# Optimization experiments

Measured on AMD Instinct MI355X. Metric: run time of the kernel, lower is better.

Reference implementation:

```python
import jax, jax.numpy as jnp
import numpy as np

B, N, INP = 16, 1024, 256
HEADS, DIM_HEAD = 8, 32
INNER = HEADS * DIM_HEAD  # 256
OUP = 256
IH = IW = 32  # IH*IW == N


def _relative_index(ih, iw):
    # mirrors the torch __init__ construction (meshgrid indexing='ij')
    coords = np.stack(np.meshgrid(np.arange(ih), np.arange(iw), indexing='ij')).reshape(2, -1)
    rel = coords[:, :, None] - coords[:, None, :]  # [2, N, N]
    rel[0] += ih - 1
    rel[1] += iw - 1
    rel[0] *= 2 * iw - 1
    return rel.sum(0).reshape(-1)  # [N*N]


def setup_inputs() -> dict:
    key = jax.random.key(0)
    kx, kqkv, kout, kbias = jax.random.split(key, 4)
    x = jax.random.normal(kx, (B, N, INP), dtype=jnp.float32)
    w_qkv = jax.random.normal(kqkv, (INP, 3 * INNER), dtype=jnp.float32) * 0.02
    w_out = jax.random.normal(kout, (INNER, OUP), dtype=jnp.float32) * 0.02
    b_out = jnp.zeros((OUP,), dtype=jnp.float32)
    bias_table = jax.random.normal(kbias, ((2 * IH - 1) * (2 * IW - 1), HEADS), dtype=jnp.float32) * 0.02
    relative_index = jnp.asarray(_relative_index(IH, IW), dtype=jnp.int32)
    return {"x": x, "w_qkv": w_qkv, "w_out": w_out, "b_out": b_out,
            "bias_table": bias_table, "relative_index": relative_index}


def reference(x, w_qkv, w_out, b_out, bias_table, relative_index):
    b, n, _ = x.shape
    scale = DIM_HEAD ** (-0.5)
    qkv = x @ w_qkv  # [b, n, 3*inner]
    q, k, v = jnp.split(qkv, 3, axis=-1)
    split_heads = lambda t: t.reshape(b, n, HEADS, DIM_HEAD).transpose(0, 2, 1, 3)  # b h n d
    q, k, v = split_heads(q), split_heads(k), split_heads(v)
    dots = jnp.einsum('bhnd,bhmd->bhnm', q, k) * scale  # [b, h, n, n]
    # gather bias: (n*n, heads) -> (1, heads, n, n), matching '(h w) c -> 1 c h w'
    rel_bias = bias_table[relative_index].reshape(n, n, HEADS).transpose(2, 0, 1)[None]
    attn = jax.nn.softmax(dots + rel_bias, axis=-1)
    out = jnp.einsum('bhnm,bhmd->bhnd', attn, v)
    out = out.transpose(0, 2, 1, 3).reshape(b, n, INNER)  # b n (h d)
    return out @ w_out + b_out
```

## Files before the change

kernel.cpp:

```cpp
#include <hip/hip_runtime.h>
#include <hip/hip_bf16.h>

typedef __bf16 bf16;
typedef bf16 bf16x4 __attribute__((ext_vector_type(4)));
typedef bf16 bf16x8 __attribute__((ext_vector_type(8)));
typedef float f32x4 __attribute__((ext_vector_type(4)));

#define MFMA32(A, B, C) __builtin_amdgcn_mfma_f32_16x16x32_bf16(A, B, C, 0, 0, 0)
#define GL2LDS16(gp, lp)                                                            \
  __builtin_amdgcn_global_load_lds((const __attribute__((address_space(1))) unsigned int*)(gp), \
                                   (__attribute__((address_space(3))) unsigned int*)(lp), 16, 0, 0)

static constexpr float SCALE = 0.17677669529663687f;
static constexpr float LOG2E = 1.4426950408889634f;

__global__ __launch_bounds__(256) void k_prep(const float* __restrict__ x,
                                              const float* __restrict__ wqkv,
                                              const float* __restrict__ wout,
                                              const float* __restrict__ table,
                                              const int* __restrict__ ridx,
                                              bf16* __restrict__ xb, bf16* __restrict__ wtq,
                                              bf16* __restrict__ wto, bf16* __restrict__ rbb) {
  const int tid = threadIdx.x;
  const int blk = blockIdx.x;
  if (blk < 2048) {
    int t = blk * 256 + tid;
    const float4* s = reinterpret_cast<const float4*>(x) + (size_t)t * 2;
    float4 a = s[0], c = s[1];
    bf16x8 o;
    o[0] = (bf16)a.x; o[1] = (bf16)a.y; o[2] = (bf16)a.z; o[3] = (bf16)a.w;
    o[4] = (bf16)c.x; o[5] = (bf16)c.y; o[6] = (bf16)c.z; o[7] = (bf16)c.w;
    reinterpret_cast<bf16x8*>(xb)[t] = o;
  } else if (blk < 3072) {
    int t = (blk - 2048) * 256 + tid;
    if (t < 196608) {
      int n = t >> 8, k = t & 255;
      wtq[t] = (bf16)wqkv[k * 768 + n];
    } else {
      int t2 = t - 196608;
      int n = t2 >> 8, k = t2 & 255;
      wto[t2] = (bf16)wout[k * 256 + n];
    }
  } else {
    const int bb2 = blk - 3072;
    const int qt = bb2 >> 6, kt = bb2 & 63;
    const int r = tid & 3, lane = tid >> 2;
    const int ln = lane & 15, quad = lane >> 4;
    const int qrow = qt * 16 + ln;
    const int key = kt * 16 + quad * 4 + r;
    const int idx = ridx[qrow * 1024 + key];
    const float4* p = reinterpret_cast<const float4*>(table) + idx * 2;
    float4 a = p[0], c = p[1];
    float vals[8] = {a.x, a.y, a.z, a.w, c.x, c.y, c.z, c.w};
    const int base = bb2 * 256 + tid;
#pragma unroll
    for (int h = 0; h < 8; ++h) rbb[h * 1048576 + base] = (bf16)(vals[h] * LOG2E);
  }
}

template <int EPI>
__global__ __launch_bounds__(256) void k_gemm(const bf16* __restrict__ A,
                                              const bf16* __restrict__ Bt,
                                              bf16* __restrict__ q, bf16* __restrict__ kk,
                                              bf16* __restrict__ vt, float* __restrict__ out,
                                              const float* __restrict__ bout) {
  __shared__ __align__(16) bf16 As[128 * 40];
  __shared__ __align__(16) bf16 Bs[128 * 40];
  const int tid = threadIdx.x;
  const int ln = tid & 15, quad = (tid >> 4) & 3, wv = tid >> 6;
  const int wm = (wv >> 1) * 64, wn = (wv & 1) * 64;
  const int m0 = blockIdx.x * 128, n0 = blockIdx.y * 128;
  const int srow = tid >> 2, scg = (tid & 3) * 8;
  f32x4 acc[4][4] = {};

  for (int kt = 0; kt < 256; kt += 32) {
    bf16x8 av0 = *reinterpret_cast<const bf16x8*>(&A[(m0 + srow) * 256 + kt + scg]);
    bf16x8 av1 = *reinterpret_cast<const bf16x8*>(&A[(m0 + 64 + srow) * 256 + kt + scg]);
    bf16x8 bv0 = *reinterpret_cast<const bf16x8*>(&Bt[(n0 + srow) * 256 + kt + scg]);
    bf16x8 bv1 = *reinterpret_cast<const bf16x8*>(&Bt[(n0 + 64 + srow) * 256 + kt + scg]);
    *reinterpret_cast<bf16x8*>(&As[srow * 40 + scg]) = av0;
    *reinterpret_cast<bf16x8*>(&As[(64 + srow) * 40 + scg]) = av1;
    *reinterpret_cast<bf16x8*>(&Bs[srow * 40 + scg]) = bv0;
    *reinterpret_cast<bf16x8*>(&Bs[(64 + srow) * 40 + scg]) = bv1;
    __syncthreads();
    bf16x8 af[4], bfr[4];
#pragma unroll
    for (int i = 0; i < 4; ++i)
      af[i] = *reinterpret_cast<const bf16x8*>(&As[(wm + i * 16 + ln) * 40 + quad * 8]);
#pragma unroll
    for (int i = 0; i < 4; ++i)
      bfr[i] = *reinterpret_cast<const bf16x8*>(&Bs[(wn + i * 16 + ln) * 40 + quad * 8]);
#pragma unroll
    for (int i = 0; i < 4; ++i)
#pragma unroll
      for (int j = 0; j < 4; ++j) acc[i][j] = MFMA32(af[i], bfr[j], acc[i][j]);
    __syncthreads();
  }

  if (EPI == 0) {
    const int colbase = n0 + wn;
    const int seg = colbase >> 8;
    const int cb = colbase & 255;
    const float mul = (seg == 0) ? SCALE * LOG2E : 1.0f;
#pragma unroll
    for (int i = 0; i < 4; ++i) {
      const int gm = m0 + wm + i * 16 + quad * 4;
      const int b = gm >> 10;
#pragma unroll
      for (int j = 0; j < 4; ++j) {
        const int gc = cb + j * 16 + ln;
        const int h = gc >> 5, d = gc & 31;
#pragma unroll
        for (int r = 0; r < 4; ++r) {
          const int nseq = (gm + r) & 1023;
          if (seg == 2) {
            const int p6 = nseq & 63;
            const int c6 = ((p6 >> 2) & 3) * 16 + (p6 >> 4) * 4 + (p6 & 3);
            const int kcol = (nseq & ~63) | c6;
            vt[(b * 8 + h) * 32768 + d * 1024 + kcol] = (bf16)acc[i][j][r];
          } else {
            bf16* dst = (seg == 0) ? q : kk;
            dst[(b * 8 + h) * 32768 + nseq * 32 + d] = (bf16)(acc[i][j][r] * mul);
          }
        }
      }
    }
  } else {
#pragma unroll
    for (int j = 0; j < 4; ++j) {
      const int gc = n0 + wn + j * 16 + ln;
      const float bb = bout[gc];
#pragma unroll
      for (int i = 0; i < 4; ++i) {
        const int gm = m0 + wm + i * 16 + quad * 4;
#pragma unroll
        for (int r = 0; r < 4; ++r) out[(size_t)(gm + r) * 256 + gc] = acc[i][j][r] + bb;
      }
    }
  }
}

__global__ __launch_bounds__(256) void k_flash(const bf16* __restrict__ qs,
                                               const bf16* __restrict__ ks,
                                               const bf16* __restrict__ vtg,
                                               const bf16* __restrict__ rbb,
                                               bf16* __restrict__ ao) {
  __shared__ __align__(16) bf16 Ks[2][2048];
  __shared__ __align__(16) bf16 Vs[2][2048];
  __shared__ __align__(16) bf16 Ps[4][16][72];
  const int tid = threadIdx.x;
  const int lane = tid & 63;
  const int ln = lane & 15, quad = lane >> 4, wv = tid >> 6;
  const int blk = blockIdx.x;
  const int bh = blk & 127;
  const int b = bh >> 3, h = bh & 7;
  const int qtw = (blk >> 7) * 4 + wv;
  const int q0 = qtw * 16;
  const bf16* qb = qs + bh * 32768;
  const bf16* kb = ks + bh * 32768;
  const bf16* vb = vtg + bh * 32768;
  const bf16* bbias = rbb + h * 1048576 + qtw * 16384 + lane * 4;

  const bf16* kg = kb + lane * 32 + wv * 8;
  const bf16* vg = vb + (lane & 31) * 1024 + (wv * 2 + (lane >> 5)) * 8;
  bf16* kls0 = &Ks[0][wv * 512];
  bf16* vls0 = &Vs[0][wv * 512];
  bf16* kls1 = &Ks[1][wv * 512];
  bf16* vls1 = &Vs[1][wv * 512];

  const bf16x8 qfrag = *reinterpret_cast<const bf16x8*>(&qb[(q0 + ln) * 32 + quad * 8]);

  f32x4 acc0 = {0.f, 0.f, 0.f, 0.f}, acc1 = {0.f, 0.f, 0.f, 0.f};
  float lsum = 0.f;

  bf16x4 cbf[2][4];
#pragma unroll
  for (int nt = 0; nt < 4; ++nt) cbf[0][nt] = *reinterpret_cast<const bf16x4*>(&bbias[nt * 256]);
  GL2LDS16(kg, kls0);
  GL2LDS16(vg, vls0);

#pragma unroll 2
  for (int it = 0; it < 16; ++it) {
    const int cur = it & 1, nxt = cur ^ 1;
    const int k0 = it * 64;
    __syncthreads();
    const int kpf = (it < 15) ? k0 + 64 : k0;
    GL2LDS16(kg + kpf * 32, cur ? kls0 : kls1);
    GL2LDS16(vg + kpf, cur ? vls0 : vls1);
#pragma unroll
    for (int nt = 0; nt < 4; ++nt)
      cbf[nxt][nt] = *reinterpret_cast<const bf16x4*>(&bbias[((it < 15 ? it + 1 : it) * 4 + nt) * 256]);
    bf16x8 kf[4];
#pragma unroll
    for (int nt = 0; nt < 4; ++nt)
      kf[nt] = *reinterpret_cast<const bf16x8*>(&Ks[cur][quad * 512 + (nt * 16 + ln) * 8]);
    f32x4 s[4];
#pragma unroll
    for (int nt = 0; nt < 4; ++nt) {
      f32x4 c;
#pragma unroll
      for (int e = 0; e < 4; ++e) c[e] = (float)cbf[cur][nt][e];
      s[nt] = MFMA32(kf[nt], qfrag, c);
    }
    bf16x8 va0 = *reinterpret_cast<const bf16x8*>(&Vs[cur][quad * 256 + ln * 8]);
    bf16x8 vc0 = *reinterpret_cast<const bf16x8*>(&Vs[cur][quad * 256 + (16 + ln) * 8]);
    bf16x8 va1 = *reinterpret_cast<const bf16x8*>(&Vs[cur][(4 + quad) * 256 + ln * 8]);
    bf16x8 vc1 = *reinterpret_cast<const bf16x8*>(&Vs[cur][(4 + quad) * 256 + (16 + ln) * 8]);
#pragma unroll
    for (int nt = 0; nt < 4; ++nt)
#pragma unroll
      for (int e = 0; e < 4; ++e) s[nt][e] = __builtin_amdgcn_exp2f(s[nt][e]);
#pragma unroll
    for (int nt = 0; nt < 4; ++nt) lsum += (s[nt][0] + s[nt][1]) + (s[nt][2] + s[nt][3]);
    bf16x8 lo, hi;
#pragma unroll
    for (int e = 0; e < 4; ++e) {
      lo[e] = (bf16)s[0][e];
      lo[4 + e] = (bf16)s[1][e];
      hi[e] = (bf16)s[2][e];
      hi[4 + e] = (bf16)s[3][e];
    }
    *reinterpret_cast<bf16x8*>(&Ps[wv][ln][quad * 16]) = lo;
    *reinterpret_cast<bf16x8*>(&Ps[wv][ln][quad * 16 + 8]) = hi;
    bf16x8 pa0 = *reinterpret_cast<const bf16x8*>(&Ps[wv][ln][quad * 8]);
    bf16x8 pa1 = *reinterpret_cast<const bf16x8*>(&Ps[wv][ln][32 + quad * 8]);
    acc0 = MFMA32(pa0, va0, acc0);
    acc1 = MFMA32(pa0, vc0, acc1);
    acc0 = MFMA32(pa1, va1, acc0);
    acc1 = MFMA32(pa1, vc1, acc1);
  }

  lsum += __shfl_xor(lsum, 16, 64);
  lsum += __shfl_xor(lsum, 32, 64);

#pragma unroll
  for (int r = 0; r < 4; ++r) {
    const float inv = __builtin_amdgcn_rcpf(__shfl(lsum, quad * 4 + r, 64));
    const int row = q0 + quad * 4 + r;
    bf16* po = &ao[(size_t)(b * 1024 + row) * 256 + h * 32 + ln];
    po[0] = (bf16)(acc0[r] * inv);
    po[16] = (bf16)(acc1[r] * inv);
  }
}

extern "C" void kernel_launch(void* const* d_in, const int* in_sizes, int n_in,
                              void* d_out, int out_size, void* d_ws, size_t ws_size,
                              hipStream_t stream) {
  const float* x = (const float*)d_in[0];
  const float* wqkv = (const float*)d_in[1];
  const float* wout = (const float*)d_in[2];
  const float* bout = (const float*)d_in[3];
  const float* btab = (const float*)d_in[4];
  const int* ridx = (const int*)d_in[5];
  float* out = (float*)d_out;

  char* ws = (char*)d_ws;
  bf16* xb  = (bf16*)(ws + 0);
  bf16* wtq = (bf16*)(ws + 8388608);
  bf16* wto = (bf16*)(ws + 8781824);
  bf16* q   = (bf16*)(ws + 8912896);
  bf16* k   = (bf16*)(ws + 17301504);
  bf16* vt  = (bf16*)(ws + 25690112);
  bf16* rb  = (bf16*)(ws + 34078720);
  bf16* ao  = (bf16*)(ws + 50855936);

  k_prep<<<7168, 256, 0, stream>>>(x, wqkv, wout, btab, ridx, xb, wtq, wto, rb);
  k_gemm<0><<<dim3(128, 6), 256, 0, stream>>>(xb, wtq, q, k, vt, nullptr, nullptr);
  k_flash<<<2048, 256, 0, stream>>>(q, k, vt, rb, ao);
  k_gemm<1><<<dim3(128, 2), 256, 0, stream>>>(ao, wto, nullptr, nullptr, nullptr, out, bout);
}
```

Before: 159.5 us.

## Double-buffer GEMM via direct global-to-LDS loads; process two query tiles per flash wave

The GEMM kernel now stages A/B tiles with global_load_lds into double-buffered shared memory without padding. This removes one barrier per step and overlaps the next tile's load with the MFMAs. The flash kernel has each wave handle two 16-row query tiles, so each K/V shared-memory fragment is reused twice, and the grid is halved. The changes raise register pressure and may add LDS bank conflicts in the unpadded GEMM layout, and the smaller grid reduces parallelism.

```diff
diff --git a/kernel.cpp b/kernel.cpp
--- a/kernel.cpp
+++ b/kernel.cpp
@@ -64,37 +64,43 @@
                                               bf16* __restrict__ q, bf16* __restrict__ kk,
                                               bf16* __restrict__ vt, float* __restrict__ out,
                                               const float* __restrict__ bout) {
-  __shared__ __align__(16) bf16 As[128 * 40];
-  __shared__ __align__(16) bf16 Bs[128 * 40];
+  __shared__ __align__(16) bf16 As[2][4096];
+  __shared__ __align__(16) bf16 Bs[2][4096];
   const int tid = threadIdx.x;
   const int ln = tid & 15, quad = (tid >> 4) & 3, wv = tid >> 6;
   const int wm = (wv >> 1) * 64, wn = (wv & 1) * 64;
   const int m0 = blockIdx.x * 128, n0 = blockIdx.y * 128;
   const int srow = tid >> 2, scg = (tid & 3) * 8;
+  const bf16* ag = A + (size_t)(m0 + srow) * 256 + scg;
+  const bf16* bg = Bt + (size_t)(n0 + srow) * 256 + scg;
   f32x4 acc[4][4] = {};
 
+  GL2LDS16(ag, &As[0][tid * 8]);
+  GL2LDS16(ag + 64 * 256, &As[0][2048 + tid * 8]);
+  GL2LDS16(bg, &Bs[0][tid * 8]);
+  GL2LDS16(bg + 64 * 256, &Bs[0][2048 + tid * 8]);
+
+#pragma unroll 2
   for (int kt = 0; kt < 256; kt += 32) {
-    bf16x8 av0 = *reinterpret_cast<const bf16x8*>(&A[(m0 + srow) * 256 + kt + scg]);
-    bf16x8 av1 = *reinterpret_cast<const bf16x8*>(&A[(m0 + 64 + srow) * 256 + kt + scg]);
-    bf16x8 bv0 = *reinterpret_cast<const bf16x8*>(&Bt[(n0 + srow) * 256 + kt + scg]);
-    bf16x8 bv1 = *reinterpret_cast<const bf16x8*>(&Bt[(n0 + 64 + srow) * 256 + kt + scg]);
-    *reinterpret_cast<bf16x8*>(&As[srow * 40 + scg]) = av0;
-    *reinterpret_cast<bf16x8*>(&As[(64 + srow) * 40 + scg]) = av1;
-    *reinterpret_cast<bf16x8*>(&Bs[srow * 40 + scg]) = bv0;
-    *reinterpret_cast<bf16x8*>(&Bs[(64 + srow) * 40 + scg]) = bv1;
+    const int cur = (kt >> 5) & 1, nxt = cur ^ 1;
     __syncthreads();
+    if (kt < 224) {
+      GL2LDS16(ag + kt + 32, &As[nxt][tid * 8]);
+      GL2LDS16(ag + 64 * 256 + kt + 32, &As[nxt][2048 + tid * 8]);
+      GL2LDS16(bg + kt + 32, &Bs[nxt][tid * 8]);
+      GL2LDS16(bg + 64 * 256 + kt + 32, &Bs[nxt][2048 + tid * 8]);
+    }
     bf16x8 af[4], bfr[4];
 #pragma unroll
     for (int i = 0; i < 4; ++i)
-      af[i] = *reinterpret_cast<const bf16x8*>(&As[(wm + i * 16 + ln) * 40 + quad * 8]);
+      af[i] = *reinterpret_cast<const bf16x8*>(&As[cur][(wm + i * 16 + ln) * 32 + quad * 8]);
 #pragma unroll
     for (int i = 0; i < 4; ++i)
-      bfr[i] = *reinterpret_cast<const bf16x8*>(&Bs[(wn + i * 16 + ln) * 40 + quad * 8]);
+      bfr[i] = *reinterpret_cast<const bf16x8*>(&Bs[cur][(wn + i * 16 + ln) * 32 + quad * 8]);
 #pragma unroll
     for (int i = 0; i < 4; ++i)
 #pragma unroll
       for (int j = 0; j < 4; ++j) acc[i][j] = MFMA32(af[i], bfr[j], acc[i][j]);
-    __syncthreads();
   }
 
   if (EPI == 0) {
@@ -147,37 +153,39 @@
                                                bf16* __restrict__ ao) {
   __shared__ __align__(16) bf16 Ks[2][2048];
   __shared__ __align__(16) bf16 Vs[2][2048];
-  __shared__ __align__(16) bf16 Ps[4][16][72];
+  __shared__ __align__(16) bf16 Ps[4][2][16][72];
   const int tid = threadIdx.x;
   const int lane = tid & 63;
   const int ln = lane & 15, quad = lane >> 4, wv = tid >> 6;
   const int blk = blockIdx.x;
   const int bh = blk & 127;
   const int b = bh >> 3, h = bh & 7;
-  const int qtw = (blk >> 7) * 4 + wv;
-  const int q0 = qtw * 16;
+  const int tA = (blk >> 7) * 8 + wv * 2;
+  const int tB = tA + 1;
   const bf16* qb = qs + bh * 32768;
   const bf16* kb = ks + bh * 32768;
   const bf16* vb = vtg + bh * 32768;
-  const bf16* bbias = rbb + h * 1048576 + qtw * 16384 + lane * 4;
+  const bf16* bbA = rbb + h * 1048576 + tA * 16384 + lane * 4;
+  const bf16* bbB = rbb + h * 1048576 + tB * 16384 + lane * 4;
 
   const bf16* kg = kb + lane * 32 + wv * 8;
   const bf16* vg = vb + (lane & 31) * 1024 + (wv * 2 + (lane >> 5)) * 8;
-  bf16* kls0 = &Ks[0][wv * 512];
-  bf16* vls0 = &Vs[0][wv * 512];
-  bf16* kls1 = &Ks[1][wv * 512];
-  bf16* vls1 = &Vs[1][wv * 512];
-
-  const bf16x8 qfrag = *reinterpret_cast<const bf16x8*>(&qb[(q0 + ln) * 32 + quad * 8]);
-
-  f32x4 acc0 = {0.f, 0.f, 0.f, 0.f}, acc1 = {0.f, 0.f, 0.f, 0.f};
-  float lsum = 0.f;
-
-  bf16x4 cbf[2][4];
-#pragma unroll
-  for (int nt = 0; nt < 4; ++nt) cbf[0][nt] = *reinterpret_cast<const bf16x4*>(&bbias[nt * 256]);
-  GL2LDS16(kg, kls0);
-  GL2LDS16(vg, vls0);
+
+  const bf16x8 qfA = *reinterpret_cast<const bf16x8*>(&qb[(tA * 16 + ln) * 32 + quad * 8]);
+  const bf16x8 qfB = *reinterpret_cast<const bf16x8*>(&qb[(tB * 16 + ln) * 32 + quad * 8]);
+
+  f32x4 accA0 = {0.f, 0.f, 0.f, 0.f}, accA1 = {0.f, 0.f, 0.f, 0.f};
+  f32x4 accB0 = {0.f, 0.f, 0.f, 0.f}, accB1 = {0.f, 0.f, 0.f, 0.f};
+  float lsA = 0.f, lsB = 0.f;
+
+  bf16x4 cbA[2][4], cbB[2][4];
+#pragma unroll
+  for (int nt = 0; nt < 4; ++nt) {
+    cbA[0][nt] = *reinterpret_cast<const bf16x4*>(&bbA[nt * 256]);
+    cbB[0][nt] = *reinterpret_cast<const bf16x4*>(&bbB[nt * 256]);
+  }
+  GL2LDS16(kg, &Ks[0][wv * 512]);
+  GL2LDS16(vg, &Vs[0][wv * 512]);
 
 #pragma unroll 2
   for (int it = 0; it < 16; ++it) {
@@ -185,22 +193,29 @@
     const int k0 = it * 64;
     __syncthreads();
     const int kpf = (it < 15) ? k0 + 64 : k0;
-    GL2LDS16(kg + kpf * 32, cur ? kls0 : kls1);
-    GL2LDS16(vg + kpf, cur ? vls0 : vls1);
-#pragma unroll
-    for (int nt = 0; nt < 4; ++nt)
-      cbf[nxt][nt] = *reinterpret_cast<const bf16x4*>(&bbias[((it < 15 ? it + 1 : it) * 4 + nt) * 256]);
+    GL2LDS16(kg + kpf * 32, &Ks[nxt][wv * 512]);
+    GL2LDS16(vg + kpf, &Vs[nxt][wv * 512]);
+    const int bnx = (it < 15 ? it + 1 : it) * 4;
+#pragma unroll
+    for (int nt = 0; nt < 4; ++nt) {
+      cbA[nxt][nt] = *reinterpret_cast<const bf16x4*>(&bbA[(bnx + nt) * 256]);
+      cbB[nxt][nt] = *reinterpret_cast<const bf16x4*>(&bbB[(bnx + nt) * 256]);
+    }
     bf16x8 kf[4];
 #pragma unroll
     for (int nt = 0; nt < 4; ++nt)
       kf[nt] = *reinterpret_cast<const bf16x8*>(&Ks[cur][quad * 512 + (nt * 16 + ln) * 8]);
-    f32x4 s[4];
+    f32x4 sA[4], sB[4];
 #pragma unroll
     for (int nt = 0; nt < 4; ++nt) {
-      f32x4 c;
-#pragma unroll
-      for (int e = 0; e < 4; ++e) c[e] = (float)cbf[cur][nt][e];
-      s[nt] = MFMA32(kf[nt], qfrag, c);
+      f32x4 cA, cB;
+#pragma unroll
+      for (int e = 0; e < 4; ++e) {
+        cA[e] = (float)cbA[cur][nt][e];
+        cB[e] = (float)cbB[cur][nt][e];
+      }
+      sA[nt] = MFMA32(kf[nt], qfA, cA);
+      sB[nt] = MFMA32(kf[nt], qfB, cB);
     }
     bf16x8 va0 = *reinterpret_cast<const bf16x8*>(&Vs[cur][quad * 256 + ln * 8]);
     bf16x8 vc0 = *reinterpret_cast<const bf16x8*>(&Vs[cur][quad * 256 + (16 + ln) * 8]);
@@ -209,37 +224,72 @@
 #pragma unroll
     for (int nt = 0; nt < 4; ++nt)
 #pragma unroll
-      for (int e = 0; e < 4; ++e) s[nt][e] = __builtin_amdgcn_exp2f(s[nt][e]);
-#pragma unroll
-    for (int nt = 0; nt < 4; ++nt) lsum += (s[nt][0] + s[nt][1]) + (s[nt][2] + s[nt][3]);
-    bf16x8 lo, hi;
-#pragma unroll
-    for (int e = 0; e < 4; ++e) {
-      lo[e] = (bf16)s[0][e];
-      lo[4 + e] = (bf16)s[1][e];
-      hi[e] = (bf16)s[2][e];
-      hi[4 + e] = (bf16)s[3][e];
-    }
-    *reinterpret_cast<bf16x8*>(&Ps[wv][ln][quad * 16]) = lo;
-    *reinterpret_cast<bf16x8*>(&Ps[wv][ln][quad * 16 + 8]) = hi;
-    bf16x8 pa0 = *reinterpret_cast<const bf16x8*>(&Ps[wv][ln][quad * 8]);
-    bf16x8 pa1 = *reinterpret_cast<const bf16x8*>(&Ps[wv][ln][32 + quad * 8]);
-    acc0 = MFMA32(pa0, va0, acc0);
-    acc1 = MFMA32(pa0, vc0, acc1);
-    acc0 = MFMA32(pa1, va1, acc0);
-    acc1 = MFMA32(pa1, vc1, acc1);
-  }
-
-  lsum += __shfl_xor(lsum, 16, 64);
-  lsum += __shfl_xor(lsum, 32, 64);
+      for (int e = 0; e < 4; ++e) sA[nt][e] = __builtin_amdgcn_exp2f(sA[nt][e]);
+#pragma unroll
+    for (int nt = 0; nt < 4; ++nt) lsA += (sA[nt][0] + sA[nt][1]) + (sA[nt][2] + sA[nt][3]);
+    {
+      bf16x8 lo, hi;
+#pragma unroll
+      for (int e = 0; e < 4; ++e) {
+        lo[e] = (bf16)sA[0][e];
+        lo[4 + e] = (bf16)sA[1][e];
+        hi[e] = (bf16)sA[2][e];
+        hi[4 + e] = (bf16)sA[3][e];
+      }
+      *reinterpret_cast<bf16x8*>(&Ps[wv][0][ln][quad * 16]) = lo;
+      *reinterpret_cast<bf16x8*>(&Ps[wv][0][ln][quad * 16 + 8]) = hi;
+    }
+#pragma unroll
+    for (int nt = 0; nt < 4; ++nt)
+#pragma unroll
+      for (int e = 0; e < 4; ++e) sB[nt][e] = __builtin_amdgcn_exp2f(sB[nt][e]);
+#pragma unroll
+    for (int nt = 0; nt < 4; ++nt) lsB += (sB[nt][0] + sB[nt][1]) + (sB[nt][2] + sB[nt][3]);
+    {
+      bf16x8 lo, hi;
+#pragma unroll
+      for (int e = 0; e < 4; ++e) {
+        lo[e] = (bf16)sB[0][e];
+        lo[4 + e] = (bf16)sB[1][e];
+        hi[e] = (bf16)sB[2][e];
+        hi[4 + e] = (bf16)sB[3][e];
+      }
+      *reinterpret_cast<bf16x8*>(&Ps[wv][1][ln][quad * 16]) = lo;
+      *reinterpret_cast<bf16x8*>(&Ps[wv][1][ln][quad * 16 + 8]) = hi;
+    }
+    {
+      bf16x8 pa0 = *reinterpret_cast<const bf16x8*>(&Ps[wv][0][ln][quad * 8]);
+      bf16x8 pa1 = *reinterpret_cast<const bf16x8*>(&Ps[wv][0][ln][32 + quad * 8]);
+      accA0 = MFMA32(pa0, va0, accA0);
+      accA1 = MFMA32(pa0, vc0, accA1);
+      accA0 = MFMA32(pa1, va1, accA0);
+      accA1 = MFMA32(pa1, vc1, accA1);
+      bf16x8 pb0 = *reinterpret_cast<const bf16x8*>(&Ps[wv][1][ln][quad * 8]);
+      bf16x8 pb1 = *reinterpret_cast<const bf16x8*>(&Ps[wv][1][ln][32 + quad * 8]);
+      accB0 = MFMA32(pb0, va0, accB0);
+      accB1 = MFMA32(pb0, vc0, accB1);
+      accB0 = MFMA32(pb1, va1, accB0);
+      accB1 = MFMA32(pb1, vc1, accB1);
+    }
+  }
+
+  lsA += __shfl_xor(lsA, 16, 64);
+  lsA += __shfl_xor(lsA, 32, 64);
+  lsB += __shfl_xor(lsB, 16, 64);
+  lsB += __shfl_xor(lsB, 32, 64);
 
 #pragma unroll
   for (int r = 0; r < 4; ++r) {
-    const float inv = __builtin_amdgcn_rcpf(__shfl(lsum, quad * 4 + r, 64));
-    const int row = q0 + quad * 4 + r;
-    bf16* po = &ao[(size_t)(b * 1024 + row) * 256 + h * 32 + ln];
-    po[0] = (bf16)(acc0[r] * inv);
-    po[16] = (bf16)(acc1[r] * inv);
+    const float invA = __builtin_amdgcn_rcpf(__shfl(lsA, quad * 4 + r, 64));
+    const int rowA = tA * 16 + quad * 4 + r;
+    bf16* poA = &ao[(size_t)(b * 1024 + rowA) * 256 + h * 32 + ln];
+    poA[0] = (bf16)(accA0[r] * invA);
+    poA[16] = (bf16)(accA1[r] * invA);
+    const float invB = __builtin_amdgcn_rcpf(__shfl(lsB, quad * 4 + r, 64));
+    const int rowB = tB * 16 + quad * 4 + r;
+    bf16* poB = &ao[(size_t)(b * 1024 + rowB) * 256 + h * 32 + ln];
+    poB[0] = (bf16)(accB0[r] * invB);
+    poB[16] = (bf16)(accB1[r] * invB);
   }
 }
 
@@ -266,6 +316,6 @@
 
   k_prep<<<7168, 256, 0, stream>>>(x, wqkv, wout, btab, ridx, xb, wtq, wto, rb);
   k_gemm<0><<<dim3(128, 6), 256, 0, stream>>>(xb, wtq, q, k, vt, nullptr, nullptr);
-  k_flash<<<2048, 256, 0, stream>>>(q, k, vt, rb, ao);
+  k_flash<<<1024, 256, 0, stream>>>(q, k, vt, rb, ao);
   k_gemm<1><<<dim3(128, 2), 256, 0, stream>>>(ao, wto, nullptr, nullptr, nullptr, out, bout);
 }
```

Result: slower. 163.8 us (+2.7%).
